# Optimization experiments

Hardware: AMD Instinct MI355X
Metric: run time of the kernel (lower is better)

Reference implementation:

```python
import jax, jax.numpy as jnp
import numpy as np


def setup_inputs() -> dict:
    key = jax.random.key(0)
    k1, k2, k3 = jax.random.split(key, 3)
    B, C, H, W = 16, 32, 48, 48
    inp = jax.random.normal(k1, (B, C, H, W), dtype=jnp.float32)
    # weight channels encode a CxC matrix per pixel; add identity (in the
    # flattened C*C channel layout) so every per-pixel matrix is well
    # conditioned for solve/slogdet, as a trained flow's weights would be.
    w = jax.random.normal(k2, (B, C * C, H, W), dtype=jnp.float32) * 0.1
    eye = jnp.eye(C, dtype=jnp.float32).reshape(C * C, 1, 1)
    w = w + eye
    logdet = jax.random.normal(k3, (B,), dtype=jnp.float32)
    return {"input": inp, "weight": w, "logdet": logdet}


def reference(input, weight, logdet):
    # forward (reverse=False) path of InvConditionalLinear
    B, C, H, W = input.shape
    # [B, C*C, H, W] -> [B, H, W, C, C] per-pixel matrices
    w = jnp.transpose(weight, (0, 2, 3, 1)).reshape(B, H, W, C, C)
    # sum of per-pixel log|det W| over all pixels -> [B]
    weight_logdet = jnp.sum(jnp.linalg.slogdet(w)[1], axis=(1, 2))
    # batched per-pixel solve: W z = x
    rhs = jnp.transpose(input, (0, 2, 3, 1))[..., None]  # [B,H,W,C,1]
    z = jnp.linalg.solve(w, rhs)[..., 0]                  # [B,H,W,C]
    z = jnp.transpose(z, (0, 3, 1, 2))                    # [B,C,H,W]
    return z, logdet - weight_logdet
```

## Files before the change

kernel.cpp:

```cpp
#include <hip/hip_runtime.h>
#include <math.h>

#define CDIM 32
#define HWDIM 2304
#define BDIM 16
#define PPW 8
#define NTHREADS 256
#define PPB 32
#define ZOFF (BDIM * CDIM * HWDIM)

__global__ __launch_bounds__(NTHREADS, 2)
void solve_kernel(const float* __restrict__ input,
                  const float* __restrict__ weight,
                  const float* __restrict__ logdet,
                  float* __restrict__ out) {
    const int t    = threadIdx.x;
    const int lane = t & 63;
    const int wv   = t >> 6;
    const int h    = lane & 7;
    const int p    = lane >> 3;
    const int gb   = lane & 56;

    const int blk  = blockIdx.x;
    const int b    = blk / (HWDIM / PPB);
    const int pb   = (blk % (HWDIM / PPB)) * PPB;
    const int pixl = wv * PPW + p;
    const int pix0 = pb + wv * PPW;
    const int pix  = pb + pixl;

    __shared__ float lds[256 * CDIM];

    const float* xp = input + (size_t)b * CDIM * HWDIM + (size_t)h * HWDIM + pix;
    float y[4];
    #pragma unroll
    for (int r = 0; r < 4; ++r) y[r] = xp[(size_t)(r * 8) * HWDIM];

    const int sg = lane >> 3;
    const int sp = lane & 7;
    const int ps = pixl >> 2, pc = pixl & 3;
    const float* wbase = weight + (size_t)b * (CDIM * CDIM) * HWDIM + pb;

    float A[4][CDIM];
    float4 v[8];

    #pragma unroll
    for (int q = 0; q < 8; ++q) {
        const int rcl = wv * 64 + q * 8 + sg;
        v[q] = *reinterpret_cast<const float4*>(wbase + (size_t)rcl * HWDIM + 4 * sp);
    }

    #pragma unroll
    for (int r = 0; r < 4; ++r) {
        if (r > 0) {
            asm volatile("s_waitcnt lgkmcnt(0)" ::: "memory");
            __builtin_amdgcn_s_barrier();
            asm volatile("" ::: "memory");
        }
        #pragma unroll
        for (int q = 0; q < 8; ++q) {
            const int rcl = wv * 64 + q * 8 + sg;
            *reinterpret_cast<float4*>(
                &lds[rcl * CDIM + ((sp ^ (rcl >> 5)) << 2)]) = v[q];
        }
        if (r < 3) {
            #pragma unroll
            for (int q = 0; q < 8; ++q) {
                const int rcl = wv * 64 + q * 8 + sg;
                v[q] = *reinterpret_cast<const float4*>(
                    wbase + (size_t)((r + 1) * 256 + rcl) * HWDIM + 4 * sp);
            }
        }
        asm volatile("s_waitcnt lgkmcnt(0)" ::: "memory");
        __builtin_amdgcn_s_barrier();
        asm volatile("" ::: "memory");
        #pragma unroll
        for (int j = 0; j < CDIM; ++j)
            A[r][j] = lds[(h * CDIM + j) * CDIM + ((ps ^ h) << 2) + pc];
    }

    float lacc = 0.0f;
    #pragma unroll
    for (int k = 0; k < CDIM; ++k) {
        const int tr = k >> 3, k7 = k & 7;
        const int src = gb + k7;
        float bp = __shfl(A[tr][k], src);
        float r  = __builtin_amdgcn_rcpf(bp);
        lacc += __log2f(fabsf(bp));

        float m[4];
        m[tr] = (h > k7) ? A[tr][k] * r : ((h == k7) ? (1.0f - r) : 0.0f);
        #pragma unroll
        for (int q = tr + 1; q < 4; ++q) m[q] = A[q][k] * r;

        #pragma unroll
        for (int j = k + 1; j < CDIM; ++j) {
            float bv = __shfl(A[tr][j], src);
            #pragma unroll
            for (int q = tr; q < 4; ++q)
                A[q][j] = fmaf(-m[q], bv, A[q][j]);
        }
        float bq = __shfl(y[tr], src);
        #pragma unroll
        for (int q = tr; q < 4; ++q) y[q] = fmaf(-m[q], bq, y[q]);
    }

    #pragma unroll
    for (int k = CDIM - 1; k >= 1; --k) {
        const int tr = k >> 3, k7 = k & 7;
        const int src = gb + k7;
        float bz = __shfl(y[tr], src);
        float c = (h < k7) ? A[tr][k] : 0.0f;
        y[tr] = fmaf(-c, bz, y[tr]);
        #pragma unroll
        for (int q = 0; q < tr; ++q)
            y[q] = fmaf(-A[q][k], bz, y[q]);
    }

    float* zp = out + (size_t)b * CDIM * HWDIM + (size_t)h * HWDIM + pix;
    #pragma unroll
    for (int r = 0; r < 4; ++r) zp[(size_t)(r * 8) * HWDIM] = y[r];

    float v2 = lacc;
    v2 += __shfl_xor(v2, 8);
    v2 += __shfl_xor(v2, 16);
    v2 += __shfl_xor(v2, 32);
    if (lane == 0) {
        float add = -v2 * 0.69314718055994531f;
        if (pix0 == 0) add += logdet[b];
        atomicAdd(&out[ZOFF + b], add);
    }
}

extern "C" void kernel_launch(void* const* d_in, const int* in_sizes, int n_in,
                              void* d_out, int out_size, void* d_ws, size_t ws_size,
                              hipStream_t stream) {
    const float* input  = (const float*)d_in[0];
    const float* weight = (const float*)d_in[1];
    const float* logdet = (const float*)d_in[2];
    float* out = (float*)d_out;

    solve_kernel<<<BDIM * (HWDIM / PPB), NTHREADS, 0, stream>>>(input, weight,
                                                                logdet, out);
}
```

Baseline: 273.8 us.

## Stream weight tiles directly into double-buffered LDS via global_load_lds

Replaces the register-staged global-to-LDS copy of per-pixel weight matrices with direct global_load_lds DMA into two LDS buffers. Loading is pipelined across four row-chunks using vmcnt waits, so the next chunk streams in while the current one is read into registers. This removes VGPR staging and the explicit ds_write traffic, but doubles the LDS footprint to 64KB per block, which may limit occupancy. The XOR swizzle now moves to the global source address so the LDS layout stays conflict-free.

After: 258.8 us. 5.5% less time.

```diff
diff --git a/kernel.cpp b/kernel.cpp
--- a/kernel.cpp
+++ b/kernel.cpp
@@ -8,6 +8,12 @@
 #define NTHREADS 256
 #define PPB 32
 #define ZOFF (BDIM * CDIM * HWDIM)
+
+__device__ __forceinline__ void gload_lds16(const float* g, float* l) {
+    __builtin_amdgcn_global_load_lds(
+        (const __attribute__((address_space(1))) float*)g,
+        (__attribute__((address_space(3))) float*)l, 16, 0, 0);
+}
 
 __global__ __launch_bounds__(NTHREADS, 2)
 void solve_kernel(const float* __restrict__ input,
@@ -28,54 +34,53 @@
     const int pix0 = pb + wv * PPW;
     const int pix  = pb + pixl;
 
-    __shared__ float lds[256 * CDIM];
+    __shared__ float lds[2][256 * CDIM];
 
     const float* xp = input + (size_t)b * CDIM * HWDIM + (size_t)h * HWDIM + pix;
     float y[4];
     #pragma unroll
     for (int r = 0; r < 4; ++r) y[r] = xp[(size_t)(r * 8) * HWDIM];
+    asm volatile("" ::: "memory");
 
     const int sg = lane >> 3;
     const int sp = lane & 7;
     const int ps = pixl >> 2, pc = pixl & 3;
     const float* wbase = weight + (size_t)b * (CDIM * CDIM) * HWDIM + pb;
+    const float* srcA = wbase + (size_t)(wv * 64 + sg) * HWDIM
+                              + ((sp ^ (2 * wv)) << 2);
+    const float* srcB = wbase + (size_t)(wv * 64 + sg) * HWDIM
+                              + ((sp ^ (2 * wv + 1)) << 2);
+
+    auto stage = [&](int r, int buf) {
+        float* lbase = &lds[buf][(wv * 64) * CDIM];
+        #pragma unroll
+        for (int q = 0; q < 8; ++q) {
+            const float* s = (q < 4 ? srcA : srcB)
+                           + (size_t)(r * 256 + q * 8) * HWDIM;
+            gload_lds16(s, lbase + q * 8 * CDIM);
+        }
+    };
+
+    stage(0, 0);
+    asm volatile("" ::: "memory");
+    stage(1, 1);
 
     float A[4][CDIM];
-    float4 v[8];
-
-    #pragma unroll
-    for (int q = 0; q < 8; ++q) {
-        const int rcl = wv * 64 + q * 8 + sg;
-        v[q] = *reinterpret_cast<const float4*>(wbase + (size_t)rcl * HWDIM + 4 * sp);
-    }
-
     #pragma unroll
     for (int r = 0; r < 4; ++r) {
-        if (r > 0) {
-            asm volatile("s_waitcnt lgkmcnt(0)" ::: "memory");
-            __builtin_amdgcn_s_barrier();
-            asm volatile("" ::: "memory");
-        }
-        #pragma unroll
-        for (int q = 0; q < 8; ++q) {
-            const int rcl = wv * 64 + q * 8 + sg;
-            *reinterpret_cast<float4*>(
-                &lds[rcl * CDIM + ((sp ^ (rcl >> 5)) << 2)]) = v[q];
-        }
-        if (r < 3) {
-            #pragma unroll
-            for (int q = 0; q < 8; ++q) {
-                const int rcl = wv * 64 + q * 8 + sg;
-                v[q] = *reinterpret_cast<const float4*>(
-                    wbase + (size_t)((r + 1) * 256 + rcl) * HWDIM + 4 * sp);
-            }
-        }
-        asm volatile("s_waitcnt lgkmcnt(0)" ::: "memory");
+        if (r < 3) asm volatile("s_waitcnt vmcnt(8)" ::: "memory");
+        else       asm volatile("s_waitcnt vmcnt(0)" ::: "memory");
         __builtin_amdgcn_s_barrier();
         asm volatile("" ::: "memory");
         #pragma unroll
         for (int j = 0; j < CDIM; ++j)
-            A[r][j] = lds[(h * CDIM + j) * CDIM + ((ps ^ h) << 2) + pc];
+            A[r][j] = lds[r & 1][(h * CDIM + j) * CDIM + ((ps ^ h) << 2) + pc];
+        if (r < 2) {
+            asm volatile("s_waitcnt lgkmcnt(0)" ::: "memory");
+            __builtin_amdgcn_s_barrier();
+            asm volatile("" ::: "memory");
+            stage(r + 2, r & 1);
+        }
     }
 
     float lacc = 0.0f;
```
